# Kernel tuning notes

Hardware: AMD Instinct MI355X
Metric: run time of the kernel (lower is better)

## Reference

```python
import jax, jax.numpy as jnp
import numpy as np

N_NODES = 50000
N_EDGES = 800000
F = 64
EPS = 1e-5


def batchnorm(x, gamma, beta):
    # training-mode BatchNorm1d: batch mean, biased variance
    mu = jnp.mean(x, axis=0)
    var = jnp.mean((x - mu) ** 2, axis=0)
    return gamma * (x - mu) * jax.lax.rsqrt(var + EPS) + beta


def setup_inputs() -> dict:
    key = jax.random.key(0)
    ks = jax.random.split(key, 10)
    s = 1.0 / np.sqrt(3 * F)
    return {
        "node_feats": jax.random.normal(ks[0], (N_NODES, F), jnp.float32),
        "edge_feats": jax.random.normal(ks[1], (N_EDGES, F), jnp.float32),
        "src": jax.random.randint(ks[2], (N_EDGES,), 0, N_NODES, jnp.int32),
        "dst": jax.random.randint(ks[3], (N_EDGES,), 0, N_NODES, jnp.int32),
        "W_mlpt": jax.random.uniform(ks[4], (3 * F, F), jnp.float32, -s, s),
        "b_mlpt": jnp.zeros((F,), jnp.float32),
        "g_mlpt": jnp.ones((F,), jnp.float32),
        "be_mlpt": jnp.zeros((F,), jnp.float32),
        "W_gate": jax.random.uniform(ks[5], (3 * F, F), jnp.float32, -s, s),
        "b_gate": jnp.zeros((F,), jnp.float32),
        "g_gate": jnp.ones((F,), jnp.float32),
        "be_gate": jnp.zeros((F,), jnp.float32),
        "g_node": jnp.ones((F,), jnp.float32),
        "be_node": jnp.zeros((F,), jnp.float32),
    }


def reference(node_feats, edge_feats, src, dst,
              W_mlpt, b_mlpt, g_mlpt, be_mlpt,
              W_gate, b_gate, g_gate, be_gate,
              g_node, be_node):
    # edge-wise gather + concat: [E, 3F]
    h_cat = jnp.concatenate(
        [node_feats[src], node_feats[dst], edge_feats], axis=1)
    # two small MLPs: Linear + BN + activation (dropout p=0)
    h_mlpt = jax.nn.sigmoid(batchnorm(h_cat @ W_mlpt + b_mlpt, g_mlpt, be_mlpt))
    h_gate = jax.nn.softplus(batchnorm(h_cat @ W_gate + b_gate, g_gate, be_gate))
    h_upd = h_mlpt * h_gate  # [E, F]
    # scatter-sum messages onto destination nodes
    agg = jax.ops.segment_sum(h_upd, dst, num_segments=N_NODES)  # [N, F]
    node_out = jax.nn.sigmoid(batchnorm(agg, g_node, be_node) + node_feats)
    return (node_out, edge_feats)
```

## Files before the change

### kernel.cpp

```cpp
#include <hip/hip_runtime.h>

#define E_TOT   800000
#define NN      50000
#define FF      64

typedef __attribute__((ext_vector_type(8))) short  short8;
typedef __attribute__((ext_vector_type(4))) float  f32x4;

__device__ __forceinline__ unsigned short f2bf(float f) {
  union { float f; unsigned int u; } v; v.f = f;
  unsigned int r = v.u + 0x7fffu + ((v.u >> 16) & 1u);
  return (unsigned short)(r >> 16);
}

__device__ __forceinline__ unsigned int pkbf(float a, float b) {
  unsigned int r;
  asm("v_cvt_pk_bf16_f32 %0, %1, %2" : "=v"(r) : "v"(a), "v"(b));
  return r;
}

__device__ __forceinline__ void atomic_pk_bf16(unsigned short* p, unsigned int v) {
  asm volatile("global_atomic_pk_add_bf16 %0, %1, off" :: "v"(p), "v"(v) : "memory");
}

__device__ __forceinline__ float bflo(unsigned int u) { return __uint_as_float(u << 16); }
__device__ __forceinline__ float bfhi(unsigned int u) { return __uint_as_float(u & 0xffff0000u); }

__device__ __forceinline__ float sigmoidf_(float x) {
  return 1.f / (1.f + __expf(-x));
}

__device__ __forceinline__ short8 cvt8(float4 f0, float4 f1) {
  uint4 u = make_uint4(pkbf(f0.x, f0.y), pkbf(f0.z, f0.w),
                       pkbf(f1.x, f1.y), pkbf(f1.z, f1.w));
  return __builtin_bit_cast(short8, u);
}

__global__ void pack_w(const float* __restrict__ Wm, const float* __restrict__ Wg,
                       unsigned short* __restrict__ Wp) {
  int t = blockIdx.x * 256 + threadIdx.x;
  if (t >= 3072) return;
  int lane = t & 63;
  int kk   = (t >> 6) % 6;
  int mnt  = t / 384;
  const float* W = (mnt >> 2) ? Wg : Wm;
  int nt  = mnt & 3;
  int col = nt * 16 + (lane & 15);
  int kb  = kk * 32 + (lane >> 4) * 8;
  #pragma unroll
  for (int j = 0; j < 8; ++j)
    Wp[t * 8 + j] = f2bf(W[(kb + j) * 64 + col]);
}

__global__ __launch_bounds__(256, 6)
void edge_gemm(const float* __restrict__ nodef, const float* __restrict__ edgef,
               const int* __restrict__ src, const int* __restrict__ dst,
               const unsigned short* __restrict__ Wp,
               float* __restrict__ stats,
               uint4* __restrict__ Yw,
               float* __restrict__ outE, int write_copy)
{
  __shared__ float red[4 * 256];

  const int tid  = threadIdx.x;
  const int w    = tid >> 6, lane = tid & 63;
  const int g    = lane >> 4, r = lane & 15;
  const int e    = blockIdx.x * 64 + w * 16 + r;

  const int s = src[e], d = dst[e];

  const float4* qs = (const float4*)(nodef + (size_t)s * 64 + g * 8);
  const float4* qd = (const float4*)(nodef + (size_t)d * 64 + g * 8);
  const float4* qe = (const float4*)(edgef + (size_t)e * 64 + g * 8);

  float4 s0 = qs[0], s1 = qs[1], s2 = qs[8], s3 = qs[9];
  float4 d0 = qd[0], d1 = qd[1], d2 = qd[8], d3 = qd[9];
  float4 e0f = qe[0], e1f = qe[1], e2f = qe[8], e3f = qe[9];

  if (write_copy) {
    float4* op = (float4*)(outE + (size_t)e * 64 + g * 8);
    op[0] = e0f; op[1] = e1f; op[8] = e2f; op[9] = e3f;
  }

  const short8 aS0 = cvt8(s0, s1),   aS1 = cvt8(s2, s3);
  const short8 aD0 = cvt8(d0, d1),   aD1 = cvt8(d2, d3);
  const short8 aE0 = cvt8(e0f, e1f), aE1 = cvt8(e2f, e3f);

  const short8* wp = (const short8*)Wp;
  f32x4 acc[8] = {};

  #pragma unroll
  for (int nt = 0; nt < 8; ++nt) {
    acc[nt] = __builtin_amdgcn_mfma_f32_16x16x32_bf16(aS0, wp[(nt * 6 + 0) * 64 + lane], acc[nt], 0, 0, 0);
    acc[nt] = __builtin_amdgcn_mfma_f32_16x16x32_bf16(aS1, wp[(nt * 6 + 1) * 64 + lane], acc[nt], 0, 0, 0);
    acc[nt] = __builtin_amdgcn_mfma_f32_16x16x32_bf16(aD0, wp[(nt * 6 + 2) * 64 + lane], acc[nt], 0, 0, 0);
    acc[nt] = __builtin_amdgcn_mfma_f32_16x16x32_bf16(aD1, wp[(nt * 6 + 3) * 64 + lane], acc[nt], 0, 0, 0);
    acc[nt] = __builtin_amdgcn_mfma_f32_16x16x32_bf16(aE0, wp[(nt * 6 + 4) * 64 + lane], acc[nt], 0, 0, 0);
    acc[nt] = __builtin_amdgcn_mfma_f32_16x16x32_bf16(aE1, wp[(nt * 6 + 5) * 64 + lane], acc[nt], 0, 0, 0);
  }

  uint4* yb = Yw + (((size_t)blockIdx.x * 4 + w) * 4) * 64 + lane;
  #pragma unroll
  for (int ntp = 0; ntp < 4; ++ntp) {
    uint4 q;
    q.x = pkbf(acc[2 * ntp][0],     acc[2 * ntp][1]);
    q.y = pkbf(acc[2 * ntp][2],     acc[2 * ntp][3]);
    q.z = pkbf(acc[2 * ntp + 1][0], acc[2 * ntp + 1][1]);
    q.w = pkbf(acc[2 * ntp + 1][2], acc[2 * ntp + 1][3]);
    yb[ntp * 64] = q;
  }

  #pragma unroll
  for (int nt = 0; nt < 8; ++nt) {
    float sv = acc[nt][0] + acc[nt][1] + acc[nt][2] + acc[nt][3];
    float qv = acc[nt][0] * acc[nt][0] + acc[nt][1] * acc[nt][1] +
               acc[nt][2] * acc[nt][2] + acc[nt][3] * acc[nt][3];
    sv += __shfl_xor(sv, 16); sv += __shfl_xor(sv, 32);
    qv += __shfl_xor(qv, 16); qv += __shfl_xor(qv, 32);
    if ((lane >> 4) == 0) {
      red[w * 256 + nt * 16 + lane]       = sv;
      red[w * 256 + 128 + nt * 16 + lane] = qv;
    }
  }
  __syncthreads();
  float v = red[tid] + red[256 + tid] + red[512 + tid] + red[768 + tid];
  atomicAdd(&stats[(blockIdx.x & 63) * 256 + tid], v);
}

__global__ void finalize_edge(const float* __restrict__ stats,
                              const float* __restrict__ g_m, const float* __restrict__ be_m,
                              const float* __restrict__ g_g, const float* __restrict__ be_g,
                              float* __restrict__ coef) {
  int c = threadIdx.x;
  float s = 0.f, q = 0.f;
  for (int sl = 0; sl < 64; ++sl) { s += stats[sl * 256 + c]; q += stats[sl * 256 + 128 + c]; }
  float mu  = s * (1.f / E_TOT);
  float var = fmaxf(q * (1.f / E_TOT) - mu * mu, 0.f);
  float g   = (c < 64) ? g_m[c]  : g_g[c - 64];
  float be  = (c < 64) ? be_m[c] : be_g[c - 64];
  float a   = g * rsqrtf(var + 1e-5f);
  coef[c]       = a;
  coef[128 + c] = be - mu * a;
}

__global__ __launch_bounds__(256)
void edge_apply(const uint4* __restrict__ Yw, const int* __restrict__ dst,
                const float* __restrict__ coef,
                unsigned short* __restrict__ aggb)
{
  const int tid = threadIdx.x;
  const int w = tid >> 6, lane = tid & 63;
  const int e0 = blockIdx.x * 64;
  const int r0 = w * 16 + ((lane >> 4) << 2);
  const int4 dn = *(const int4*)&dst[e0 + r0];
  const int colb = lane & 15;
  const int par  = colb & 1;

  const uint4* yb = Yw + (((size_t)blockIdx.x * 4 + w) * 4) * 64 + lane;
  uint4 qm0 = yb[0], qm1 = yb[64], qg0 = yb[128], qg1 = yb[192];
  const unsigned int um[8] = {qm0.x, qm0.y, qm0.z, qm0.w, qm1.x, qm1.y, qm1.z, qm1.w};
  const unsigned int ug[8] = {qg0.x, qg0.y, qg0.z, qg0.w, qg1.x, qg1.y, qg1.z, qg1.w};
  const int dr[4] = {dn.x, dn.y, dn.z, dn.w};

  #pragma unroll
  for (int ntm = 0; ntm < 4; ++ntm) {
    const int col = ntm * 16 + colb;
    const float am = coef[col],      cm = coef[128 + col];
    const float ag = coef[64 + col], cg = coef[192 + col];
    float hv[4];
    #pragma unroll
    for (int p = 0; p < 2; ++p) {
      unsigned int m = um[ntm * 2 + p], g = ug[ntm * 2 + p];
      #pragma unroll
      for (int h = 0; h < 2; ++h) {
        float mv = h ? bfhi(m) : bflo(m);
        float gv = h ? bfhi(g) : bflo(g);
        float ym = fmaf(mv, am, cm);
        float yg = fmaf(gv, ag, cg);
        float sig = sigmoidf_(ym);
        float sp  = (yg > 20.f) ? yg : __logf(1.f + __expf(yg));
        hv[2 * p + h] = sig * sp;
      }
    }
    float pv[4];
    #pragma unroll
    for (int rr = 0; rr < 4; ++rr) pv[rr] = __shfl_xor(hv[rr], 1);
    const int colp = ntm * 16 + (colb & ~1);
    #pragma unroll
    for (int rr = 0; rr < 2; ++rr) {
      int rx = par * 2 + rr;
      float lo = par ? pv[rx] : hv[rx];
      float hi = par ? hv[rx] : pv[rx];
      atomic_pk_bf16(&aggb[(size_t)dr[rx] * 64 + colp], pkbf(lo, hi));
    }
  }
}

__global__ void node_stats(const unsigned int* __restrict__ aggu, float* __restrict__ nstats) {
  __shared__ float rs0[256], rq0[256], rs1[256], rq1[256];
  int tid = threadIdx.x;
  int cp = tid & 31;
  float s0 = 0.f, q0 = 0.f, s1 = 0.f, q1 = 0.f;
  for (int r = blockIdx.x * 8 + (tid >> 5); r < NN; r += gridDim.x * 8) {
    unsigned int u = aggu[r * 32 + cp];
    float v0 = bflo(u), v1 = bfhi(u);
    s0 += v0; q0 += v0 * v0; s1 += v1; q1 += v1 * v1;
  }
  rs0[tid] = s0; rq0[tid] = q0; rs1[tid] = s1; rq1[tid] = q1;
  __syncthreads();
  if (tid < 32) {
    s0 = 0.f; q0 = 0.f; s1 = 0.f; q1 = 0.f;
    #pragma unroll
    for (int k = 0; k < 8; ++k) {
      s0 += rs0[tid + 32 * k]; q0 += rq0[tid + 32 * k];
      s1 += rs1[tid + 32 * k]; q1 += rq1[tid + 32 * k];
    }
    int slot = blockIdx.x & 31;
    atomicAdd(&nstats[slot * 128 + 2 * tid],      s0);
    atomicAdd(&nstats[slot * 128 + 2 * tid + 1],  s1);
    atomicAdd(&nstats[slot * 128 + 64 + 2 * tid],     q0);
    atomicAdd(&nstats[slot * 128 + 64 + 2 * tid + 1], q1);
  }
}

__global__ void finalize_node(const float* __restrict__ nstats,
                              const float* __restrict__ g_n, const float* __restrict__ be_n,
                              float* __restrict__ coefn) {
  int c = threadIdx.x;
  float s = 0.f, q = 0.f;
  for (int sl = 0; sl < 32; ++sl) { s += nstats[sl * 128 + c]; q += nstats[sl * 128 + 64 + c]; }
  float mu  = s * (1.f / NN);
  float var = fmaxf(q * (1.f / NN) - mu * mu, 0.f);
  float a   = g_n[c] * rsqrtf(var + 1e-5f);
  coefn[c]      = a;
  coefn[64 + c] = be_n[c] - mu * a;
}

__global__ void node_out_k(float* __restrict__ out, const unsigned int* __restrict__ aggu,
                           const float* __restrict__ nodef, const float* __restrict__ coefn) {
  int i  = blockIdx.x * 256 + threadIdx.x;
  int cb = (i & 15) * 4;
  uint2  u  = ((const uint2*)aggu)[i];
  float4 nf = ((const float4*)nodef)[i];
  float4 r;
  r.x = sigmoidf_(coefn[cb + 0] * bflo(u.x) + coefn[64 + cb + 0] + nf.x);
  r.y = sigmoidf_(coefn[cb + 1] * bfhi(u.x) + coefn[64 + cb + 1] + nf.y);
  r.z = sigmoidf_(coefn[cb + 2] * bflo(u.y) + coefn[64 + cb + 2] + nf.z);
  r.w = sigmoidf_(coefn[cb + 3] * bfhi(u.y) + coefn[64 + cb + 3] + nf.w);
  ((float4*)out)[i] = r;
}

extern "C" void kernel_launch(void* const* d_in, const int* in_sizes, int n_in,
                              void* d_out, int out_size, void* d_ws, size_t ws_size,
                              hipStream_t stream) {
  const float* nodef = (const float*)d_in[0];
  const float* edgef = (const float*)d_in[1];
  const int*   src   = (const int*)d_in[2];
  const int*   dst   = (const int*)d_in[3];
  const float* W_m   = (const float*)d_in[4];
  const float* g_m   = (const float*)d_in[6];
  const float* be_m  = (const float*)d_in[7];
  const float* W_g   = (const float*)d_in[8];
  const float* g_g   = (const float*)d_in[10];
  const float* be_g  = (const float*)d_in[11];
  const float* g_n   = (const float*)d_in[12];
  const float* be_n  = (const float*)d_in[13];

  float* out  = (float*)d_out;
  float* outE = out + (size_t)NN * FF;

  char* ws = (char*)d_ws;
  unsigned short* aggb = (unsigned short*)ws;
  float* stats  = (float*)(ws + 0x640000);
  float* coef   = (float*)(ws + 0x650000);
  float* nstats = (float*)(ws + 0x651000);
  float* coefn  = (float*)(ws + 0x655000);
  unsigned short* Wp = (unsigned short*)(ws + 0x656000);

  const size_t y_bytes = (size_t)E_TOT * 128 * 2;
  const int y_in_ws = (ws_size >= (size_t)0x700000 + y_bytes);
  uint4* Yw = y_in_ws ? (uint4*)(ws + 0x700000) : (uint4*)outE;

  hipMemsetAsync(aggb, 0, (size_t)NN * FF * 2, stream);
  hipMemsetAsync(stats, 0, 0x15200, stream);

  pack_w<<<12, 256, 0, stream>>>(W_m, W_g, Wp);
  edge_gemm<<<E_TOT / 64, 256, 0, stream>>>(nodef, edgef, src, dst, Wp,
                                            stats, Yw, outE, y_in_ws);
  finalize_edge<<<1, 128, 0, stream>>>(stats, g_m, be_m, g_g, be_g, coef);
  edge_apply<<<E_TOT / 64, 256, 0, stream>>>(Yw, dst, coef, aggb);
  if (!y_in_ws) {
    hipMemcpyAsync(outE, edgef, (size_t)E_TOT * FF * sizeof(float),
                   hipMemcpyDeviceToDevice, stream);
  }
  node_stats<<<512, 256, 0, stream>>>((const unsigned int*)aggb, nstats);
  finalize_node<<<1, 64, 0, stream>>>(nstats, g_n, be_n, coefn);
  node_out_k<<<NN * FF / 4 / 256, 256, 0, stream>>>(out, (const unsigned int*)aggb,
                                                    nodef, coefn);
}
```

Baseline: 430.6 us.

## Pre-convert node features to bf16, use nontemporal streams, multi-tile edge_apply

Adds a small kernel that converts node features to bf16 once, so the edge GEMM gathers half as many bytes per src/dst row. Edge feature loads, the output copy and the intermediate Y writes and reads use nontemporal loads and stores to keep streaming data from evicting gathered node rows in cache. edge_apply now handles 10 tiles per block with double-buffered register prefetch to overlap loads with the activation math and atomics. Occupancy hints change as well. The costs are an extra launch, more workspace and higher register pressure.

After: 426.9 us. Within noise of the previous version (-0.9%).

```diff
diff --git a/kernel.cpp b/kernel.cpp
--- a/kernel.cpp
+++ b/kernel.cpp
@@ -6,6 +6,7 @@
 
 typedef __attribute__((ext_vector_type(8))) short  short8;
 typedef __attribute__((ext_vector_type(4))) float  f32x4;
+typedef __attribute__((ext_vector_type(4))) unsigned int u32x4;
 
 __device__ __forceinline__ unsigned short f2bf(float f) {
   union { float f; unsigned int u; } v; v.f = f;
@@ -30,10 +31,35 @@
   return 1.f / (1.f + __expf(-x));
 }
 
+__device__ __forceinline__ f32x4 nt_load_f4(const float* p) {
+  return __builtin_nontemporal_load((const f32x4*)p);
+}
+__device__ __forceinline__ void nt_store_f4(float* p, f32x4 v) {
+  __builtin_nontemporal_store(v, (f32x4*)p);
+}
+__device__ __forceinline__ u32x4 nt_load_u4(const unsigned int* p) {
+  return __builtin_nontemporal_load((const u32x4*)p);
+}
+__device__ __forceinline__ void nt_store_u4(unsigned int* p, u32x4 v) {
+  __builtin_nontemporal_store(v, (u32x4*)p);
+}
+
 __device__ __forceinline__ short8 cvt8(float4 f0, float4 f1) {
   uint4 u = make_uint4(pkbf(f0.x, f0.y), pkbf(f0.z, f0.w),
                        pkbf(f1.x, f1.y), pkbf(f1.z, f1.w));
   return __builtin_bit_cast(short8, u);
+}
+__device__ __forceinline__ short8 cvt8e(f32x4 f0, f32x4 f1) {
+  u32x4 u;
+  u.x = pkbf(f0.x, f0.y); u.y = pkbf(f0.z, f0.w);
+  u.z = pkbf(f1.x, f1.y); u.w = pkbf(f1.z, f1.w);
+  return __builtin_bit_cast(short8, u);
+}
+
+__global__ void cvt_node(const float2* __restrict__ nf, unsigned int* __restrict__ nb) {
+  int i = blockIdx.x * 256 + threadIdx.x;
+  float2 v = nf[i];
+  nb[i] = pkbf(v.x, v.y);
 }
 
 __global__ void pack_w(const float* __restrict__ Wm, const float* __restrict__ Wg,
@@ -52,12 +78,14 @@
     Wp[t * 8 + j] = f2bf(W[(kb + j) * 64 + col]);
 }
 
-__global__ __launch_bounds__(256, 6)
-void edge_gemm(const float* __restrict__ nodef, const float* __restrict__ edgef,
+template <int NB>
+__global__ __launch_bounds__(256, 8)
+void edge_gemm(const float* __restrict__ nodef, const unsigned short* __restrict__ nodeb,
+               const float* __restrict__ edgef,
                const int* __restrict__ src, const int* __restrict__ dst,
                const unsigned short* __restrict__ Wp,
                float* __restrict__ stats,
-               uint4* __restrict__ Yw,
+               unsigned int* __restrict__ Yw,
                float* __restrict__ outE, int write_copy)
 {
   __shared__ float red[4 * 256];
@@ -69,22 +97,32 @@
 
   const int s = src[e], d = dst[e];
 
-  const float4* qs = (const float4*)(nodef + (size_t)s * 64 + g * 8);
-  const float4* qd = (const float4*)(nodef + (size_t)d * 64 + g * 8);
-  const float4* qe = (const float4*)(edgef + (size_t)e * 64 + g * 8);
-
-  float4 s0 = qs[0], s1 = qs[1], s2 = qs[8], s3 = qs[9];
-  float4 d0 = qd[0], d1 = qd[1], d2 = qd[8], d3 = qd[9];
-  float4 e0f = qe[0], e1f = qe[1], e2f = qe[8], e3f = qe[9];
+  short8 aS0, aS1, aD0, aD1;
+  if constexpr (NB) {
+    const unsigned short* ns = nodeb + (size_t)s * 64 + g * 8;
+    const unsigned short* nd = nodeb + (size_t)d * 64 + g * 8;
+    aS0 = *(const short8*)ns;        aS1 = *(const short8*)(ns + 32);
+    aD0 = *(const short8*)nd;        aD1 = *(const short8*)(nd + 32);
+  } else {
+    const float4* qs = (const float4*)(nodef + (size_t)s * 64 + g * 8);
+    const float4* qd = (const float4*)(nodef + (size_t)d * 64 + g * 8);
+    float4 s0 = qs[0], s1 = qs[1], s2 = qs[8], s3 = qs[9];
+    float4 d0 = qd[0], d1 = qd[1], d2 = qd[8], d3 = qd[9];
+    aS0 = cvt8(s0, s1); aS1 = cvt8(s2, s3);
+    aD0 = cvt8(d0, d1); aD1 = cvt8(d2, d3);
+  }
+
+  const float* pe = edgef + (size_t)e * 64 + g * 8;
+  f32x4 e0f = nt_load_f4(pe),      e1f = nt_load_f4(pe + 4);
+  f32x4 e2f = nt_load_f4(pe + 32), e3f = nt_load_f4(pe + 36);
 
   if (write_copy) {
-    float4* op = (float4*)(outE + (size_t)e * 64 + g * 8);
-    op[0] = e0f; op[1] = e1f; op[8] = e2f; op[9] = e3f;
-  }
-
-  const short8 aS0 = cvt8(s0, s1),   aS1 = cvt8(s2, s3);
-  const short8 aD0 = cvt8(d0, d1),   aD1 = cvt8(d2, d3);
-  const short8 aE0 = cvt8(e0f, e1f), aE1 = cvt8(e2f, e3f);
+    float* op = outE + (size_t)e * 64 + g * 8;
+    nt_store_f4(op, e0f);      nt_store_f4(op + 4, e1f);
+    nt_store_f4(op + 32, e2f); nt_store_f4(op + 36, e3f);
+  }
+
+  const short8 aE0 = cvt8e(e0f, e1f), aE1 = cvt8e(e2f, e3f);
 
   const short8* wp = (const short8*)Wp;
   f32x4 acc[8] = {};
@@ -99,15 +137,15 @@
     acc[nt] = __builtin_amdgcn_mfma_f32_16x16x32_bf16(aE1, wp[(nt * 6 + 5) * 64 + lane], acc[nt], 0, 0, 0);
   }
 
-  uint4* yb = Yw + (((size_t)blockIdx.x * 4 + w) * 4) * 64 + lane;
+  unsigned int* yb = Yw + ((((size_t)blockIdx.x * 4 + w) * 4) * 64 + lane) * 4;
   #pragma unroll
   for (int ntp = 0; ntp < 4; ++ntp) {
-    uint4 q;
+    u32x4 q;
     q.x = pkbf(acc[2 * ntp][0],     acc[2 * ntp][1]);
     q.y = pkbf(acc[2 * ntp][2],     acc[2 * ntp][3]);
     q.z = pkbf(acc[2 * ntp + 1][0], acc[2 * ntp + 1][1]);
     q.w = pkbf(acc[2 * ntp + 1][2], acc[2 * ntp + 1][3]);
-    yb[ntp * 64] = q;
+    nt_store_u4(yb + ntp * 64 * 4, q);
   }
 
   #pragma unroll
@@ -143,57 +181,86 @@
   coef[128 + c] = be - mu * a;
 }
 
-__global__ __launch_bounds__(256)
-void edge_apply(const uint4* __restrict__ Yw, const int* __restrict__ dst,
+#define TPB 10
+__global__ __launch_bounds__(256, 6)
+void edge_apply(const unsigned int* __restrict__ Yw, const int* __restrict__ dst,
                 const float* __restrict__ coef,
                 unsigned short* __restrict__ aggb)
 {
   const int tid = threadIdx.x;
   const int w = tid >> 6, lane = tid & 63;
-  const int e0 = blockIdx.x * 64;
   const int r0 = w * 16 + ((lane >> 4) << 2);
-  const int4 dn = *(const int4*)&dst[e0 + r0];
   const int colb = lane & 15;
   const int par  = colb & 1;
-
-  const uint4* yb = Yw + (((size_t)blockIdx.x * 4 + w) * 4) * 64 + lane;
-  uint4 qm0 = yb[0], qm1 = yb[64], qg0 = yb[128], qg1 = yb[192];
-  const unsigned int um[8] = {qm0.x, qm0.y, qm0.z, qm0.w, qm1.x, qm1.y, qm1.z, qm1.w};
-  const unsigned int ug[8] = {qg0.x, qg0.y, qg0.z, qg0.w, qg1.x, qg1.y, qg1.z, qg1.w};
-  const int dr[4] = {dn.x, dn.y, dn.z, dn.w};
-
+  const int t0 = blockIdx.x * TPB;
+
+  float am[4], cm[4], ag[4], cg[4];
   #pragma unroll
   for (int ntm = 0; ntm < 4; ++ntm) {
     const int col = ntm * 16 + colb;
-    const float am = coef[col],      cm = coef[128 + col];
-    const float ag = coef[64 + col], cg = coef[192 + col];
-    float hv[4];
-    #pragma unroll
-    for (int p = 0; p < 2; ++p) {
-      unsigned int m = um[ntm * 2 + p], g = ug[ntm * 2 + p];
-      #pragma unroll
-      for (int h = 0; h < 2; ++h) {
-        float mv = h ? bfhi(m) : bflo(m);
-        float gv = h ? bfhi(g) : bflo(g);
-        float ym = fmaf(mv, am, cm);
-        float yg = fmaf(gv, ag, cg);
-        float sig = sigmoidf_(ym);
-        float sp  = (yg > 20.f) ? yg : __logf(1.f + __expf(yg));
-        hv[2 * p + h] = sig * sp;
-      }
-    }
-    float pv[4];
-    #pragma unroll
-    for (int rr = 0; rr < 4; ++rr) pv[rr] = __shfl_xor(hv[rr], 1);
-    const int colp = ntm * 16 + (colb & ~1);
-    #pragma unroll
-    for (int rr = 0; rr < 2; ++rr) {
-      int rx = par * 2 + rr;
-      float lo = par ? pv[rx] : hv[rx];
-      float hi = par ? hv[rx] : pv[rx];
-      atomic_pk_bf16(&aggb[(size_t)dr[rx] * 64 + colp], pkbf(lo, hi));
-    }
-  }
+    am[ntm] = coef[col];      cm[ntm] = coef[128 + col];
+    ag[ntm] = coef[64 + col]; cg[ntm] = coef[192 + col];
+  }
+
+#define LOADT(i, DN, M0, M1, G0, G1)                                            \
+  {                                                                             \
+    const int te = (t0 + (i)) * 64;                                             \
+    DN = *(const int4*)&dst[te + r0];                                           \
+    const unsigned int* yb =                                                    \
+        Yw + ((((size_t)(t0 + (i)) * 4 + w) * 4) * 64 + lane) * 4;              \
+    M0 = nt_load_u4(yb);            M1 = nt_load_u4(yb + 64 * 4);               \
+    G0 = nt_load_u4(yb + 128 * 4);  G1 = nt_load_u4(yb + 192 * 4);              \
+  }
+
+#define COMPT(DN, M0, M1, G0, G1)                                               \
+  {                                                                             \
+    const unsigned int um[8] = {M0.x, M0.y, M0.z, M0.w, M1.x, M1.y, M1.z, M1.w};\
+    const unsigned int ug[8] = {G0.x, G0.y, G0.z, G0.w, G1.x, G1.y, G1.z, G1.w};\
+    const int dr[4] = {DN.x, DN.y, DN.z, DN.w};                                 \
+    _Pragma("unroll")                                                           \
+    for (int ntm = 0; ntm < 4; ++ntm) {                                         \
+      float hv[4];                                                              \
+      _Pragma("unroll")                                                         \
+      for (int p = 0; p < 2; ++p) {                                             \
+        unsigned int m = um[ntm * 2 + p], gg = ug[ntm * 2 + p];                 \
+        _Pragma("unroll")                                                       \
+        for (int h = 0; h < 2; ++h) {                                           \
+          float mv = h ? bfhi(m) : bflo(m);                                     \
+          float gv = h ? bfhi(gg) : bflo(gg);                                   \
+          float ym = fmaf(mv, am[ntm], cm[ntm]);                                \
+          float yg = fmaf(gv, ag[ntm], cg[ntm]);                                \
+          float sig = sigmoidf_(ym);                                            \
+          float sp  = (yg > 20.f) ? yg : __logf(1.f + __expf(yg));              \
+          hv[2 * p + h] = sig * sp;                                             \
+        }                                                                       \
+      }                                                                         \
+      float pv[4];                                                              \
+      _Pragma("unroll")                                                         \
+      for (int rr = 0; rr < 4; ++rr) pv[rr] = __shfl_xor(hv[rr], 1);            \
+      const int colp = ntm * 16 + (colb & ~1);                                  \
+      _Pragma("unroll")                                                         \
+      for (int rr = 0; rr < 2; ++rr) {                                          \
+        int rx = par * 2 + rr;                                                  \
+        float lo = par ? pv[rx] : hv[rx];                                       \
+        float hi = par ? hv[rx] : pv[rx];                                       \
+        atomic_pk_bf16(&aggb[(size_t)dr[rx] * 64 + colp], pkbf(lo, hi));        \
+      }                                                                         \
+    }                                                                           \
+  }
+
+  int4 dnA, dnB;
+  u32x4 mA0, mA1, gA0, gA1, mB0, mB1, gB0, gB1;
+
+  LOADT(0, dnA, mA0, mA1, gA0, gA1)
+  #pragma unroll
+  for (int i = 0; i < TPB; i += 2) {
+    if (i + 1 < TPB) LOADT(i + 1, dnB, mB0, mB1, gB0, gB1)
+    COMPT(dnA, mA0, mA1, gA0, gA1)
+    if (i + 2 < TPB) LOADT(i + 2, dnA, mA0, mA1, gA0, gA1)
+    if (i + 1 < TPB) COMPT(dnB, mB0, mB1, gB0, gB1)
+  }
+#undef LOADT
+#undef COMPT
 }
 
 __global__ void node_stats(const unsigned int* __restrict__ aggu, float* __restrict__ nstats) {
@@ -279,16 +346,26 @@
 
   const size_t y_bytes = (size_t)E_TOT * 128 * 2;
   const int y_in_ws = (ws_size >= (size_t)0x700000 + y_bytes);
-  uint4* Yw = y_in_ws ? (uint4*)(ws + 0x700000) : (uint4*)outE;
+  unsigned int* Yw = y_in_ws ? (unsigned int*)(ws + 0x700000) : (unsigned int*)outE;
+
+  const size_t nb_off = y_in_ws ? ((size_t)0x700000 + y_bytes) : (size_t)0x700000;
+  const int use_nb = (ws_size >= nb_off + (size_t)NN * FF * 2);
+  unsigned short* nodeb = (unsigned short*)(ws + nb_off);
 
   hipMemsetAsync(aggb, 0, (size_t)NN * FF * 2, stream);
   hipMemsetAsync(stats, 0, 0x15200, stream);
 
   pack_w<<<12, 256, 0, stream>>>(W_m, W_g, Wp);
-  edge_gemm<<<E_TOT / 64, 256, 0, stream>>>(nodef, edgef, src, dst, Wp,
-                                            stats, Yw, outE, y_in_ws);
+  if (use_nb) {
+    cvt_node<<<NN * 32 / 256, 256, 0, stream>>>((const float2*)nodef, (unsigned int*)nodeb);
+    edge_gemm<1><<<E_TOT / 64, 256, 0, stream>>>(nodef, nodeb, edgef, src, dst, Wp,
+                                                 stats, Yw, outE, y_in_ws);
+  } else {
+    edge_gemm<0><<<E_TOT / 64, 256, 0, stream>>>(nodef, nodeb, edgef, src, dst, Wp,
+                                                 stats, Yw, outE, y_in_ws);
+  }
   finalize_edge<<<1, 128, 0, stream>>>(stats, g_m, be_m, g_g, be_g, coef);
-  edge_apply<<<E_TOT / 64, 256, 0, stream>>>(Yw, dst, coef, aggb);
+  edge_apply<<<E_TOT / 64 / TPB, 256, 0, stream>>>(Yw, dst, coef, aggb);
   if (!y_in_ws) {
     hipMemcpyAsync(outE, edgef, (size_t)E_TOT * FF * sizeof(float),
                    hipMemcpyDeviceToDevice, stream);
```
